# Kernel tuning notes

Measured on AMD Instinct MI355X. Metric: run time of the kernel, lower is better.

## Reference

```python
import jax, jax.numpy as jnp
import numpy as np

MARGIN = 1.0
EPS = 1e-12  # safe sqrt/normalize clamp; used entries have magnitude >> EPS


def _normalize(x):
    return x / jnp.maximum(jnp.linalg.norm(x, axis=-1, keepdims=True), EPS)


def _cdist(x, y):
    # Pairwise L2 distances, matches torch.cdist(p=2)
    sq = (jnp.sum(x * x, axis=-1)[:, None]
          + jnp.sum(y * y, axis=-1)[None, :]
          - 2.0 * (x @ y.T))
    return jnp.sqrt(jnp.maximum(sq, EPS))


def setup_inputs() -> dict:
    key = jax.random.key(0)
    k1, k2, k3 = jax.random.split(key, 3)
    B, P, D = 4096, 2, 256
    anchor = jax.random.normal(k1, (B, D), dtype=jnp.float32)
    positive = jax.random.normal(k2, (B, P, D), dtype=jnp.float32)
    labels = jax.random.randint(k3, (B,), 0, 200)
    return {"anchor": anchor, "positive": positive, "labels": labels}


def reference(anchor, positive, labels):
    a = _normalize(anchor)            # [B, D]
    p = _normalize(positive)          # [B, P, D]
    B = a.shape[0]
    all_labels = jnp.concatenate([labels, labels])           # [2B]
    neg_mask = all_labels[None, :] != labels[:, None]        # [B, 2B]
    idx = jnp.arange(B)
    losses = []
    for v in range(p.shape[1]):  # loop over small fixed num_positives
        feats = jnp.concatenate([a, p[:, v]], axis=0)        # [2B, D]
        dist = _cdist(feats, feats)                          # [2B, 2B]
        pos_dist = dist[idx, idx + B]                        # [B]
        # hard negative mining: min distance over different-label columns
        neg_dist = jnp.min(jnp.where(neg_mask, dist[:B], jnp.inf), axis=1)  # [B]
        losses.append(jnp.maximum(pos_dist - neg_dist + MARGIN, 0.0))
    return jnp.mean(jnp.stack(losses))
```

## Files before the change

kernel.cpp:

```cpp
#include <hip/hip_runtime.h>
#include <hip/hip_bf16.h>

#define NB    4096
#define ND    256
#define NP    2
#define TOT   (NB * 3)
#define NCHUNK 48
#define COLS_PER_CHUNK 256
#define TILES 16
#define NEG_INIT (-4.0f)
#define IMIN_SENT (-1073741824)
#define INV_SCALE (1.0f / 16129.0f)

typedef float f32x4 __attribute__((ext_vector_type(4)));
typedef int   i32x4 __attribute__((ext_vector_type(4)));

#define WS_F_OFF    0
#define WS_POS_OFF  (TOT * 256)
#define WS_PART_OFF (WS_POS_OFF + NB * NP * 4)

__global__ void norm_pos_kernel(const float* __restrict__ anchor,
                                const float* __restrict__ positive,
                                unsigned char* __restrict__ F2,
                                float* __restrict__ posArr) {
    int wid = threadIdx.x >> 6, lane = threadIdx.x & 63;
    int row = blockIdx.x * 4 + wid;
    int group = row >> 4, r15 = row & 15;
    int kk = lane >> 4, quad = (lane >> 2) & 3, jj = (lane & 3) * 4;
    int* dst = (int*)(F2 + (size_t)group * 4096 + kk * 1024 + (quad * 16 + r15) * 16 + jj);

    if (row < NB) {
        const float* src = anchor + (size_t)row * ND;
        float4 x = *(const float4*)(src + lane * 4);
        float ss = x.x * x.x + x.y * x.y + x.z * x.z + x.w * x.w;
        #pragma unroll
        for (int m = 1; m < 64; m <<= 1) ss += __shfl_xor(ss, m, 64);
        float inv = 127.0f / fmaxf(sqrtf(ss), 1e-12f);
        int b0 = (int)rintf(x.x * inv) & 0xff;
        int b1 = (int)rintf(x.y * inv) & 0xff;
        int b2 = (int)rintf(x.z * inv) & 0xff;
        int b3 = (int)rintf(x.w * inv) & 0xff;
        *dst = b0 | (b1 << 8) | (b2 << 16) | (b3 << 24);
    } else {
        int q = row - NB;
        int v = q >> 12;
        int j = q & (NB - 1);
        const float* sp = positive + (size_t)(j * NP + v) * ND;
        const float* sa = anchor + (size_t)j * ND;
        float4 xp = *(const float4*)(sp + lane * 4);
        float4 xa = *(const float4*)(sa + lane * 4);
        float sspv = xp.x * xp.x + xp.y * xp.y + xp.z * xp.z + xp.w * xp.w;
        float ssa  = xa.x * xa.x + xa.y * xa.y + xa.z * xa.z + xa.w * xa.w;
        float dot  = xa.x * xp.x + xa.y * xp.y + xa.z * xp.z + xa.w * xp.w;
        #pragma unroll
        for (int m = 1; m < 64; m <<= 1) {
            sspv += __shfl_xor(sspv, m, 64);
            ssa  += __shfl_xor(ssa, m, 64);
            dot  += __shfl_xor(dot, m, 64);
        }
        float invp = 127.0f / fmaxf(sqrtf(sspv), 1e-12f);
        int b0 = (int)rintf(xp.x * invp) & 0xff;
        int b1 = (int)rintf(xp.y * invp) & 0xff;
        int b2 = (int)rintf(xp.z * invp) & 0xff;
        int b3 = (int)rintf(xp.w * invp) & 0xff;
        *dst = b0 | (b1 << 8) | (b2 << 16) | (b3 << 24);
        if (lane == 0) {
            float inva = 1.0f / fmaxf(sqrtf(ssa), 1e-12f);
            float invpf = invp * (1.0f / 127.0f);
            float dn = dot * inva * invpf;
            float sq = 2.0f - 2.0f * dn;
            posArr[j * NP + v] = sqrtf(fmaxf(sq, 1e-12f));
        }
    }
}

__global__ __launch_bounds__(512) void gram_max_kernel(
        const unsigned char* __restrict__ F2,
        const int* __restrict__ labels,
        float* __restrict__ partials) {
    __shared__ unsigned char ldsB[TILES * 4096];
    __shared__ int slab[COLS_PER_CHUNK];
    int tid = threadIdx.x;
    int wid = tid >> 6, lane = tid & 63;
    int l15 = lane & 15, quad = lane >> 4;

    int id = blockIdx.x;
    int chunk = id >> 4;
    int rbi   = id & 15;

    int rowBase = rbi * 256 + wid * 32;
    int col0 = chunk * COLS_PER_CHUNK;
    int part = chunk >> 4;

    i32x4 af[2][4];
    #pragma unroll
    for (int s = 0; s < 2; ++s) {
        const unsigned char* ab = F2 + (size_t)(rbi * 16 + wid * 2 + s) * 4096 + lane * 16;
        #pragma unroll
        for (int kk = 0; kk < 4; ++kk)
            af[s][kk] = *(const i32x4*)(ab + kk * 1024);
    }
    unsigned rlp[2];
    #pragma unroll
    for (int s = 0; s < 2; ++s) {
        const int* lb = labels + rowBase + s * 16 + quad * 4;
        rlp[s] = (unsigned)lb[0] | ((unsigned)lb[1] << 8)
               | ((unsigned)lb[2] << 16) | ((unsigned)lb[3] << 24);
    }
    if (tid < COLS_PER_CHUNK) slab[tid] = labels[(col0 & (NB - 1)) + tid];

    {
        const float4* src = (const float4*)(F2 + (size_t)chunk * 16 * 4096);
        float4* dst = (float4*)ldsB;
        #pragma unroll
        for (int j = 0; j < 8; ++j)
            dst[tid + j * 512] = src[tid + j * 512];
    }

    int vmax[2][4];
    #pragma unroll
    for (int s = 0; s < 2; ++s)
        #pragma unroll
        for (int r = 0; r < 4; ++r) vmax[s][r] = IMIN_SENT;

    __syncthreads();

    #pragma unroll 2
    for (int ct = 0; ct < TILES; ++ct) {
        i32x4 bfr[4];
        #pragma unroll
        for (int kk = 0; kk < 4; ++kk)
            bfr[kk] = *(const i32x4*)&ldsB[ct * 4096 + kk * 1024 + lane * 16];

        int lc = slab[ct * 16 + l15];
        unsigned lcq = (unsigned)lc * 0x01010101u;

        i32x4 acc[2];
        #pragma unroll
        for (int s = 0; s < 2; ++s) acc[s] = (i32x4){0, 0, 0, 0};
        #pragma unroll
        for (int kk = 0; kk < 4; ++kk)
            #pragma unroll
            for (int s = 0; s < 2; ++s)
                acc[s] = __builtin_amdgcn_mfma_i32_16x16x64_i8(af[s][kk], bfr[kk], acc[s], 0, 0, 0);

        #pragma unroll
        for (int s = 0; s < 2; ++s) {
            unsigned x = rlp[s] ^ lcq;
            #pragma unroll
            for (int r = 0; r < 4; ++r) {
                bool neq = ((x >> (8 * r)) & 0xffu) != 0u;
                int cand = neq ? acc[s][r] : IMIN_SENT;
                vmax[s][r] = vmax[s][r] > cand ? vmax[s][r] : cand;
            }
        }
    }

    #pragma unroll
    for (int m = 1; m < 16; m <<= 1)
        #pragma unroll
        for (int s = 0; s < 2; ++s)
            #pragma unroll
            for (int r = 0; r < 4; ++r) {
                int o = __shfl_xor(vmax[s][r], m, 64);
                vmax[s][r] = vmax[s][r] > o ? vmax[s][r] : o;
            }

    if (l15 == 0) {
        #pragma unroll
        for (int s = 0; s < 2; ++s)
            #pragma unroll
            for (int r = 0; r < 4; ++r) {
                int row = rowBase + s * 16 + quad * 4 + r;
                partials[(size_t)part * NB * 16 + (size_t)row * 16 + (chunk & 15)]
                    = (float)vmax[s][r] * INV_SCALE;
            }
    }
}

__global__ void finalize_kernel(const float* __restrict__ partials,
                                const float* __restrict__ posArr,
                                float* __restrict__ out) {
    int row = blockIdx.x * 256 + threadIdx.x;
    const float* pa = partials + (size_t)row * 16;
    const float* pb = pa + (size_t)NB * 16;
    const float* pc = pb + (size_t)NB * 16;
    float ma = NEG_INIT, m0 = NEG_INIT, m1 = NEG_INIT;
    #pragma unroll
    for (int j = 0; j < 16; ++j) {
        ma = fmaxf(ma, pa[j]);
        m0 = fmaxf(m0, pb[j]);
        m1 = fmaxf(m1, pc[j]);
    }
    float n0 = sqrtf(fmaxf(2.0f - 2.0f * fmaxf(ma, m0), 1e-12f));
    float n1 = sqrtf(fmaxf(2.0f - 2.0f * fmaxf(ma, m1), 1e-12f));
    float l = fmaxf(posArr[row * 2 + 0] - n0 + 1.0f, 0.0f)
            + fmaxf(posArr[row * 2 + 1] - n1 + 1.0f, 0.0f);
    int lane = threadIdx.x & 63, wid = threadIdx.x >> 6;
    #pragma unroll
    for (int m = 1; m < 64; m <<= 1) l += __shfl_xor(l, m, 64);
    __shared__ float wsum[4];
    if (lane == 0) wsum[wid] = l;
    __syncthreads();
    if (threadIdx.x == 0) {
        float s = wsum[0] + wsum[1] + wsum[2] + wsum[3];
        atomicAdd(out, s * (1.0f / (NB * NP)));
    }
}

extern "C" void kernel_launch(void* const* d_in, const int* in_sizes, int n_in,
                              void* d_out, int out_size, void* d_ws, size_t ws_size,
                              hipStream_t stream) {
    const float* anchor   = (const float*)d_in[0];
    const float* positive = (const float*)d_in[1];
    const int*   labels   = (const int*)d_in[2];
    float* out = (float*)d_out;

    unsigned char* F2 = (unsigned char*)((char*)d_ws + WS_F_OFF);
    float* posArr     = (float*)((char*)d_ws + WS_POS_OFF);
    float* partials   = (float*)((char*)d_ws + WS_PART_OFF);

    norm_pos_kernel<<<TOT / 4, 256, 0, stream>>>(anchor, positive, F2, posArr);
    gram_max_kernel<<<(NB / 256) * NCHUNK, 512, 0, stream>>>(F2, labels, partials);
    hipMemsetAsync(d_out, 0, sizeof(float), stream);
    finalize_kernel<<<NB / 256, 256, 0, stream>>>(partials, posArr, out);
}
```

Baseline: 86.77 us.

## Double-buffer column tiles in gram kernel with persistent row fragments across units

Each block now processes three 128-column units instead of one 256-column chunk, keeping its A fragments and labels in registers and prefetching the next unit's B tile into registers while computing the current one, then writing it to a second LDS buffer. Grid size drops to 512 blocks and the partial-max array grows to 32 slots per part, with finalize reading accordingly. The aim is to hide global-load latency behind MFMA work and amortize per-block setup; it adds more partial writes and fewer blocks to balance across CUs.

```diff
diff --git a/kernel.cpp b/kernel.cpp
--- a/kernel.cpp
+++ b/kernel.cpp
@@ -5,9 +5,6 @@
 #define ND    256
 #define NP    2
 #define TOT   (NB * 3)
-#define NCHUNK 48
-#define COLS_PER_CHUNK 256
-#define TILES 16
 #define NEG_INIT (-4.0f)
 #define IMIN_SENT (-1073741824)
 #define INV_SCALE (1.0f / 16129.0f)
@@ -78,19 +75,17 @@
         const unsigned char* __restrict__ F2,
         const int* __restrict__ labels,
         float* __restrict__ partials) {
-    __shared__ unsigned char ldsB[TILES * 4096];
-    __shared__ int slab[COLS_PER_CHUNK];
+    __shared__ unsigned char ldsB[2 * 32768];
+    __shared__ int slab[384];
     int tid = threadIdx.x;
     int wid = tid >> 6, lane = tid & 63;
     int l15 = lane & 15, quad = lane >> 4;
 
     int id = blockIdx.x;
-    int chunk = id >> 4;
-    int rbi   = id & 15;
+    int rbi    = id & 15;
+    int cgroup = id >> 4;
 
     int rowBase = rbi * 256 + wid * 32;
-    int col0 = chunk * COLS_PER_CHUNK;
-    int part = chunk >> 4;
 
     i32x4 af[2][4];
     #pragma unroll
@@ -107,74 +102,91 @@
         rlp[s] = (unsigned)lb[0] | ((unsigned)lb[1] << 8)
                | ((unsigned)lb[2] << 16) | ((unsigned)lb[3] << 24);
     }
-    if (tid < COLS_PER_CHUNK) slab[tid] = labels[(col0 & (NB - 1)) + tid];
-
-    {
-        const float4* src = (const float4*)(F2 + (size_t)chunk * 16 * 4096);
-        float4* dst = (float4*)ldsB;
-        #pragma unroll
-        for (int j = 0; j < 8; ++j)
-            dst[tid + j * 512] = src[tid + j * 512];
-    }
-
-    int vmax[2][4];
-    #pragma unroll
-    for (int s = 0; s < 2; ++s)
-        #pragma unroll
-        for (int r = 0; r < 4; ++r) vmax[s][r] = IMIN_SENT;
-
+    if (tid < 384) slab[tid] = labels[(cgroup * 384 + tid) & (NB - 1)];
+
+    float4 bt[4];
+    auto gloadU = [&](int u) {
+        const float4* s = (const float4*)(F2 + (size_t)(cgroup * 3 + u) * 32768);
+        #pragma unroll
+        for (int j = 0; j < 4; ++j) bt[j] = s[tid + j * 512];
+    };
+    auto swriteU = [&](int buf) {
+        float4* d = (float4*)(ldsB + buf * 32768);
+        #pragma unroll
+        for (int j = 0; j < 4; ++j) d[tid + j * 512] = bt[j];
+    };
+
+    gloadU(0); swriteU(0);
+    gloadU(1);
     __syncthreads();
 
-    #pragma unroll 2
-    for (int ct = 0; ct < TILES; ++ct) {
-        i32x4 bfr[4];
-        #pragma unroll
-        for (int kk = 0; kk < 4; ++kk)
-            bfr[kk] = *(const i32x4*)&ldsB[ct * 4096 + kk * 1024 + lane * 16];
-
-        int lc = slab[ct * 16 + l15];
-        unsigned lcq = (unsigned)lc * 0x01010101u;
-
-        i32x4 acc[2];
-        #pragma unroll
-        for (int s = 0; s < 2; ++s) acc[s] = (i32x4){0, 0, 0, 0};
-        #pragma unroll
-        for (int kk = 0; kk < 4; ++kk)
+    for (int u = 0; u < 3; ++u) {
+        int buf = u & 1;
+        int c = cgroup * 3 + u;
+        int part = c >> 5;
+
+        int vmax[2][4];
+        #pragma unroll
+        for (int s = 0; s < 2; ++s)
+            #pragma unroll
+            for (int r = 0; r < 4; ++r) vmax[s][r] = IMIN_SENT;
+
+        #pragma unroll 2
+        for (int ct = 0; ct < 8; ++ct) {
+            i32x4 bfr[4];
+            #pragma unroll
+            for (int kk = 0; kk < 4; ++kk)
+                bfr[kk] = *(const i32x4*)&ldsB[buf * 32768 + ct * 4096 + kk * 1024 + lane * 16];
+
+            int lc = slab[u * 128 + ct * 16 + l15];
+            unsigned lcq = (unsigned)lc * 0x01010101u;
+
+            i32x4 acc[2];
+            #pragma unroll
+            for (int s = 0; s < 2; ++s) acc[s] = (i32x4){0, 0, 0, 0};
+            #pragma unroll
+            for (int kk = 0; kk < 4; ++kk)
+                #pragma unroll
+                for (int s = 0; s < 2; ++s)
+                    acc[s] = __builtin_amdgcn_mfma_i32_16x16x64_i8(af[s][kk], bfr[kk], acc[s], 0, 0, 0);
+
+            #pragma unroll
+            for (int s = 0; s < 2; ++s) {
+                unsigned x = rlp[s] ^ lcq;
+                #pragma unroll
+                for (int r = 0; r < 4; ++r) {
+                    bool neq = ((x >> (8 * r)) & 0xffu) != 0u;
+                    int cand = neq ? acc[s][r] : IMIN_SENT;
+                    vmax[s][r] = vmax[s][r] > cand ? vmax[s][r] : cand;
+                }
+            }
+        }
+
+        #pragma unroll
+        for (int m = 1; m < 16; m <<= 1)
             #pragma unroll
             for (int s = 0; s < 2; ++s)
-                acc[s] = __builtin_amdgcn_mfma_i32_16x16x64_i8(af[s][kk], bfr[kk], acc[s], 0, 0, 0);
-
-        #pragma unroll
-        for (int s = 0; s < 2; ++s) {
-            unsigned x = rlp[s] ^ lcq;
-            #pragma unroll
-            for (int r = 0; r < 4; ++r) {
-                bool neq = ((x >> (8 * r)) & 0xffu) != 0u;
-                int cand = neq ? acc[s][r] : IMIN_SENT;
-                vmax[s][r] = vmax[s][r] > cand ? vmax[s][r] : cand;
-            }
-        }
-    }
-
-    #pragma unroll
-    for (int m = 1; m < 16; m <<= 1)
-        #pragma unroll
-        for (int s = 0; s < 2; ++s)
-            #pragma unroll
-            for (int r = 0; r < 4; ++r) {
-                int o = __shfl_xor(vmax[s][r], m, 64);
-                vmax[s][r] = vmax[s][r] > o ? vmax[s][r] : o;
-            }
-
-    if (l15 == 0) {
-        #pragma unroll
-        for (int s = 0; s < 2; ++s)
-            #pragma unroll
-            for (int r = 0; r < 4; ++r) {
-                int row = rowBase + s * 16 + quad * 4 + r;
-                partials[(size_t)part * NB * 16 + (size_t)row * 16 + (chunk & 15)]
-                    = (float)vmax[s][r] * INV_SCALE;
-            }
+                #pragma unroll
+                for (int r = 0; r < 4; ++r) {
+                    int o = __shfl_xor(vmax[s][r], m, 64);
+                    vmax[s][r] = vmax[s][r] > o ? vmax[s][r] : o;
+                }
+        if (l15 == 0) {
+            #pragma unroll
+            for (int s = 0; s < 2; ++s)
+                #pragma unroll
+                for (int r = 0; r < 4; ++r) {
+                    int row = rowBase + s * 16 + quad * 4 + r;
+                    partials[(size_t)part * NB * 32 + (size_t)row * 32 + (c & 31)]
+                        = (float)vmax[s][r] * INV_SCALE;
+                }
+        }
+
+        if (u < 2) {
+            swriteU(buf ^ 1);
+            if (u == 0) gloadU(2);
+            __syncthreads();
+        }
     }
 }
 
@@ -182,12 +194,12 @@
                                 const float* __restrict__ posArr,
                                 float* __restrict__ out) {
     int row = blockIdx.x * 256 + threadIdx.x;
-    const float* pa = partials + (size_t)row * 16;
-    const float* pb = pa + (size_t)NB * 16;
-    const float* pc = pb + (size_t)NB * 16;
+    const float* pa = partials + (size_t)row * 32;
+    const float* pb = pa + (size_t)NB * 32;
+    const float* pc = pb + (size_t)NB * 32;
     float ma = NEG_INIT, m0 = NEG_INIT, m1 = NEG_INIT;
     #pragma unroll
-    for (int j = 0; j < 16; ++j) {
+    for (int j = 0; j < 32; ++j) {
         ma = fmaxf(ma, pa[j]);
         m0 = fmaxf(m0, pb[j]);
         m1 = fmaxf(m1, pc[j]);
@@ -220,8 +232,8 @@
     float* posArr     = (float*)((char*)d_ws + WS_POS_OFF);
     float* partials   = (float*)((char*)d_ws + WS_PART_OFF);
 
+    hipMemsetAsync(d_out, 0, sizeof(float), stream);
     norm_pos_kernel<<<TOT / 4, 256, 0, stream>>>(anchor, positive, F2, posArr);
-    gram_max_kernel<<<(NB / 256) * NCHUNK, 512, 0, stream>>>(F2, labels, partials);
-    hipMemsetAsync(d_out, 0, sizeof(float), stream);
+    gram_max_kernel<<<512, 512, 0, stream>>>(F2, labels, partials);
     finalize_kernel<<<NB / 256, 256, 0, stream>>>(partials, posArr, out);
 }
```

After: 95.85 us. +10.5%, slower.
